# Performance work log

Measured on AMD Instinct MI355X. Metric: run time of the kernel, lower is better.

Reference implementation:

```python
import jax, jax.numpy as jnp
import numpy as np

NH = 8          # n_heads
CLIP = 10.0     # tanh_clipping


def _make_heads(x):
    # (B, n, H) -> (B, NH, n, H//NH)
    B, n, H = x.shape
    return x.reshape(B, n, NH, H // NH).transpose(0, 2, 1, 3)


def setup_inputs() -> dict:
    key = jax.random.key(0)
    ks = jax.random.split(key, 12)
    B, N, G, H = 64, 2000, 128, 128
    s = 1.0 / np.sqrt(H)
    embeddings = jax.random.normal(ks[0], (B, N, H), jnp.float32)
    u = jax.random.uniform(ks[1], (B, G, N))
    group_ninf_mask = jnp.where(u < 0.1, -1e9, 0.0).astype(jnp.float32)
    w = lambda k: (jax.random.normal(k, (H, H), jnp.float32) * s)
    return {
        'embeddings': embeddings,
        'group_ninf_mask': group_ninf_mask,
        'Wq_graph': w(ks[2]), 'Wq_source': w(ks[3]), 'Wq_target': w(ks[4]),
        'Wq_last': w(ks[5]), 'Wk': w(ks[6]), 'Wv': w(ks[7]),
        'Wc': w(ks[8]), 'bc': jnp.zeros((H,), jnp.float32),
        'source_node': jax.random.randint(ks[9], (B,), 0, N),
        'target_node': jax.random.randint(ks[10], (B,), 0, N),
        'last_node': jax.random.randint(ks[11], (B, G), 0, N),
    }


def reference(embeddings, group_ninf_mask, Wq_graph, Wq_source, Wq_target,
              Wq_last, Wk, Wv, Wc, bc, source_node, target_node, last_node):
    B, N, H = embeddings.shape
    G = group_ninf_mask.shape[1]
    hd = H // NH
    b = jnp.arange(B)

    # --- reset() state ---
    graph_emb = embeddings.mean(axis=1, keepdims=True)              # (B,1,H)
    q_graph = _make_heads(graph_emb @ Wq_graph.T)                   # (B,NH,1,hd)
    src_emb = embeddings[b, source_node][:, None, :]                # (B,1,H)
    q_source = _make_heads(src_emb @ Wq_source.T)
    tgt_emb = embeddings[b, target_node][:, None, :]                # (B,1,H)
    q_target = _make_heads(tgt_emb @ Wq_target.T)
    glimpse_k = _make_heads(embeddings @ Wk.T)                      # (B,NH,N,hd)
    glimpse_v = _make_heads(embeddings @ Wv.T)                      # (B,NH,N,hd)

    # --- forward(last_node) ---
    last_emb = embeddings[b[:, None], last_node]                    # (B,G,H)
    q_last = _make_heads(last_emb @ Wq_last.T)                      # (B,NH,G,hd)
    glimpse_q = q_graph + q_source + q_target + q_last              # (B,NH,G,hd)

    scores = jnp.einsum('bhgd,bhnd->bhgn', glimpse_q, glimpse_k) / np.sqrt(hd)
    scores = scores + group_ninf_mask[:, None, :, :]                # mask per head
    attn = jax.nn.softmax(scores, axis=-1)                          # (B,NH,G,N)
    heads = jnp.einsum('bhgn,bhnd->bhgd', attn, glimpse_v)          # (B,NH,G,hd)
    mh_out = heads.transpose(0, 2, 1, 3).reshape(B, G, H)           # (B,G,H)
    final_q = mh_out @ Wc.T + bc                                    # multi_head_combine

    # single-head logits vs logit_k = embeddings^T, tanh-clipped + masked
    logits = jnp.einsum('bgh,bnh->bgn', final_q, embeddings) / np.sqrt(H)
    logits = CLIP * jnp.tanh(logits) + group_ninf_mask
    probs = jax.nn.softmax(logits, axis=2)                          # (B,G,N)
    return probs
```

## Files before the change

### kernel.cpp

```cpp
#include <hip/hip_runtime.h>
#include <hip/hip_bf16.h>

#define BB 64
#define NN 2000
#define GG 128
#define HH 128
#define NHEAD 8
#define HD 16

typedef __attribute__((ext_vector_type(8))) short short8;
typedef __attribute__((ext_vector_type(4))) float f32x4;

__device__ __forceinline__ unsigned short bf16hi(float f) {
    union { float f; unsigned u; } v; v.f = f;
    return (unsigned short)(v.u >> 16);
}
__device__ __forceinline__ float bf16tof(unsigned short h) {
    union { float f; unsigned u; } v; v.u = ((unsigned)h) << 16;
    return v.f;
}

__device__ __forceinline__ void fma8x8(const float4& a0, const float4& a1,
                                       const float4& b0, const float4& b1,
                                       float acc[8][8]) {
    const float av[8] = {a0.x, a0.y, a0.z, a0.w, a1.x, a1.y, a1.z, a1.w};
    const float bv[8] = {b0.x, b0.y, b0.z, b0.w, b1.x, b1.y, b1.z, b1.w};
#pragma unroll
    for (int i = 0; i < 8; ++i)
#pragma unroll
        for (int k = 0; k < 8; ++k) acc[i][k] += av[i] * bv[k];
}

__global__ __launch_bounds__(256) void k_wt(const float* w0, const float* w1, const float* w2,
                     const float* w3, const float* w4, const float* w5,
                     const float* w6, float* WT,
                     unsigned short* Wkhi, unsigned short* Wklo,
                     unsigned short* Wvhi, unsigned short* Wvlo) {
    int m = blockIdx.x;
    if (m >= 5) {
        const float* src = (m == 5) ? w4 : w5;
        unsigned short* dh = (m == 5) ? Wkhi : Wvhi;
        unsigned short* dl = (m == 5) ? Wklo : Wvlo;
        for (int e = threadIdx.x * 4; e < 16384; e += 1024) {
            float4 v = *(const float4*)(src + e);
            float fv[4] = {v.x, v.y, v.z, v.w};
            unsigned short h4[4], l4[4];
#pragma unroll
            for (int i = 0; i < 4; ++i) {
                h4[i] = bf16hi(fv[i]); l4[i] = bf16hi(fv[i] - bf16tof(h4[i]));
            }
            uint2 ph, pl;
            ph.x = h4[0] | (h4[1] << 16); ph.y = h4[2] | (h4[3] << 16);
            pl.x = l4[0] | (l4[1] << 16); pl.y = l4[2] | (l4[3] << 16);
            *(uint2*)(dh + e) = ph;
            *(uint2*)(dl + e) = pl;
        }
        return;
    }
    __shared__ float t[128 * 129];
    const float* src = (m == 0) ? w0 : (m == 1) ? w1 : (m == 2) ? w2 : (m == 3) ? w3 : w6;
    int slot = (m == 4) ? 6 : m;
    for (int e = threadIdx.x; e < 16384; e += 256) {
        int c = e >> 7, j = e & 127;
        t[c * 129 + j] = src[e];
    }
    __syncthreads();
    for (int e = threadIdx.x; e < 16384; e += 256) {
        int j = e >> 7, c = e & 127;
        WT[slot * 16384 + e] = t[c * 129 + j];
    }
}

__global__ __launch_bounds__(256) void k_maskbits(const float* mask, unsigned long long* bits) {
    int bg = blockIdx.x;
    int lane = threadIdx.x & 63;
    int wv = threadIdx.x >> 6;
    for (int w = wv; w < 32; w += 4) {
        int n = w * 64 + lane;
        bool keep = false;
        if (n < NN) keep = (mask[(size_t)bg * NN + n] == 0.0f);
        unsigned long long bal = __ballot(keep);
        if (lane == 0) bits[bg * 32 + w] = bal;
    }
}

__global__ __launch_bounds__(128) void k_gsum(const float* emb, float* gpart) {
    int ck = blockIdx.x, b = blockIdx.y, c = threadIdx.x;
    const float* p = emb + ((size_t)b * NN + ck * 125) * HH + c;
    float s = 0.0f;
#pragma unroll 5
    for (int r = 0; r < 125; ++r) s += p[(size_t)r * HH];
    gpart[ck * 8192 + b * 128 + c] = s;
}

__global__ __launch_bounds__(128) void k_qbase(const float* emb, const int* srcn, const int* tgtn,
                        const float* gpart, const float* WT, float* qbase) {
    int b = blockIdx.x, c = threadIdx.x;
    __shared__ float ge[128], se[128], te[128];
    float s = 0.0f;
#pragma unroll
    for (int t = 0; t < 16; ++t) s += gpart[t * 8192 + b * 128 + c];
    ge[c] = s * (1.0f / 2000.0f);
    se[c] = emb[((size_t)b * NN + srcn[b]) * HH + c];
    te[c] = emb[((size_t)b * NN + tgtn[b]) * HH + c];
    __syncthreads();
    const float* Wg = WT;
    const float* Ws = WT + 16384;
    const float* Wt2 = WT + 32768;
    float acc = 0.0f;
#pragma unroll 4
    for (int j = 0; j < 128; ++j) {
        acc += ge[j] * Wg[j * 128 + c] + se[j] * Ws[j * 128 + c] + te[j] * Wt2[j * 128 + c];
    }
    qbase[b * 128 + c] = acc;
}

__global__ __launch_bounds__(256) void k_qlast(const float* emb, const int* lastn, const float* WT,
                        const float* qbase, unsigned short* Qhi, unsigned short* Qlo) {
    int b = blockIdx.x;
    int tid = threadIdx.x, xq = tid & 15, yq = tid >> 4;
    __shared__ float Bl[128 * 132];
    for (int e = tid; e < 16384; e += 256) {
        int g = e >> 7, j = e & 127;
        Bl[j * 132 + g] = emb[((size_t)b * NN + lastn[b * 128 + g]) * HH + j];
    }
    __syncthreads();
    const float* Wql = WT + 3 * 16384;
    float acc[8][8] = {};
#pragma unroll 4
    for (int j = 0; j < 128; ++j) {
        const float4* Ar = (const float4*)(Wql + j * 128);
        float4 a0 = Ar[yq], a1 = Ar[16 + yq];
        const float4* Br = (const float4*)(Bl + j * 132);
        float4 b0 = Br[xq], b1 = Br[16 + xq];
        fma8x8(a0, a1, b0, b1, acc);
    }
    float4 qb0 = *(const float4*)(qbase + b * 128 + 4 * yq);
    float4 qb1 = *(const float4*)(qbase + b * 128 + 64 + 4 * yq);
    const float q0v[4] = {qb0.x, qb0.y, qb0.z, qb0.w};
    const float q1v[4] = {qb1.x, qb1.y, qb1.z, qb1.w};
#pragma unroll
    for (int k = 0; k < 8; ++k) {
        int g = (k < 4) ? (4 * xq + k) : (64 + 4 * xq + (k - 4));
        size_t base = ((size_t)b * 128 + g) * 128;
        unsigned short h4[4], l4[4];
#pragma unroll
        for (int i = 0; i < 4; ++i) {
            float f = (acc[i][k] + q0v[i]) * 0.25f;
            h4[i] = bf16hi(f); l4[i] = bf16hi(f - bf16tof(h4[i]));
        }
        uint2 ph, pl;
        ph.x = h4[0] | (h4[1] << 16); ph.y = h4[2] | (h4[3] << 16);
        pl.x = l4[0] | (l4[1] << 16); pl.y = l4[2] | (l4[3] << 16);
        *(uint2*)(Qhi + base + 4 * yq) = ph;
        *(uint2*)(Qlo + base + 4 * yq) = pl;
#pragma unroll
        for (int i = 0; i < 4; ++i) {
            float f = (acc[4 + i][k] + q1v[i]) * 0.25f;
            h4[i] = bf16hi(f); l4[i] = bf16hi(f - bf16tof(h4[i]));
        }
        ph.x = h4[0] | (h4[1] << 16); ph.y = h4[2] | (h4[3] << 16);
        pl.x = l4[0] | (l4[1] << 16); pl.y = l4[2] | (l4[3] << 16);
        *(uint2*)(Qhi + base + 64 + 4 * yq) = ph;
        *(uint2*)(Qlo + base + 64 + 4 * yq) = pl;
    }
}

__device__ __forceinline__ void stage_emb(const float* emb, int b, int n0, int tid,
                                          unsigned short (*Eh)[128], unsigned short (*El)[128]) {
    int rr = tid >> 5, c4 = (tid & 31) * 4;
#pragma unroll
    for (int p = 0; p < 16; ++p) {
        int r = p * 8 + rr;
        int n = n0 + r;
        float4 v = make_float4(0.f, 0.f, 0.f, 0.f);
        if (n < NN) v = *(const float4*)(emb + ((size_t)b * NN + n) * HH + c4);
        float fv[4] = {v.x, v.y, v.z, v.w};
        unsigned short h4[4], l4[4];
#pragma unroll
        for (int i = 0; i < 4; ++i) {
            h4[i] = bf16hi(fv[i]); l4[i] = bf16hi(fv[i] - bf16tof(h4[i]));
        }
        uint2 ph, pl;
        ph.x = h4[0] | (h4[1] << 16); ph.y = h4[2] | (h4[3] << 16);
        pl.x = l4[0] | (l4[1] << 16); pl.y = l4[2] | (l4[3] << 16);
        int cs = c4 ^ ((r & 7) << 3);
        *(uint2*)&Eh[r][cs] = ph;
        *(uint2*)&El[r][cs] = pl;
    }
}

__global__ __launch_bounds__(256) void k_kv(const float* emb,
        const unsigned short* Wkhi, const unsigned short* Wklo,
        const unsigned short* Wvhi, const unsigned short* Wvlo,
        unsigned short* Khi, unsigned short* Klo,
        unsigned short* Vhi, unsigned short* Vlo) {
    int nt = blockIdx.x, b = blockIdx.y;
    int tid = threadIdx.x;
    int wv = tid >> 6, lane = tid & 63, l15 = lane & 15, q3 = lane >> 4;
    int n0 = nt * 128;
    __shared__ __align__(16) char ldsbuf[65536];
    unsigned short (*Eh)[128] = (unsigned short(*)[128])ldsbuf;
    unsigned short (*El)[128] = (unsigned short(*)[128])(ldsbuf + 32768);
    stage_emb(emb, b, n0, tid, Eh, El);
    __syncthreads();
    f32x4 aK[2][8], aV[2][8];
#pragma unroll
    for (int t = 0; t < 2; ++t)
#pragma unroll
        for (int ct = 0; ct < 8; ++ct) {
            aK[t][ct] = (f32x4){0.f, 0.f, 0.f, 0.f};
            aV[t][ct] = (f32x4){0.f, 0.f, 0.f, 0.f};
        }
#pragma unroll
    for (int ks = 0; ks < 4; ++ks) {
        short8 eh[2], el[2];
#pragma unroll
        for (int t = 0; t < 2; ++t) {
            int r = wv * 32 + t * 16 + l15;
            int cs = (ks * 32 + q3 * 8) ^ ((r & 7) << 3);
            eh[t] = *(const short8*)&Eh[r][cs];
            el[t] = *(const short8*)&El[r][cs];
        }
#pragma unroll
        for (int ct = 0; ct < 8; ++ct) {
            size_t woff = ((size_t)(ct * 16 + l15)) * 128 + ks * 32 + q3 * 8;
            short8 wkh = *(const short8*)(Wkhi + woff);
            short8 wkl = *(const short8*)(Wklo + woff);
            short8 wvh = *(const short8*)(Wvhi + woff);
            short8 wvl = *(const short8*)(Wvlo + woff);
#pragma unroll
            for (int t = 0; t < 2; ++t) {
                aK[t][ct] = __builtin_amdgcn_mfma_f32_16x16x32_bf16(eh[t], wkh, aK[t][ct], 0, 0, 0);
                aK[t][ct] = __builtin_amdgcn_mfma_f32_16x16x32_bf16(el[t], wkh, aK[t][ct], 0, 0, 0);
                aK[t][ct] = __builtin_amdgcn_mfma_f32_16x16x32_bf16(eh[t], wkl, aK[t][ct], 0, 0, 0);
                aV[t][ct] = __builtin_amdgcn_mfma_f32_16x16x32_bf16(eh[t], wvh, aV[t][ct], 0, 0, 0);
                aV[t][ct] = __builtin_amdgcn_mfma_f32_16x16x32_bf16(el[t], wvh, aV[t][ct], 0, 0, 0);
                aV[t][ct] = __builtin_amdgcn_mfma_f32_16x16x32_bf16(eh[t], wvl, aV[t][ct], 0, 0, 0);
            }
        }
    }
#pragma unroll
    for (int t = 0; t < 2; ++t) {
        int nb = n0 + wv * 32 + t * 16 + 4 * q3;
#pragma unroll
        for (int ct = 0; ct < 8; ++ct) {
            size_t kbase = ((size_t)b * 8 + ct) * 32000 + l15;
#pragma unroll
            for (int r = 0; r < 4; ++r) {
                int n = nb + r;
                if (n < NN) {
                    float f = aK[t][ct][r];
                    unsigned short hh = bf16hi(f);
                    Khi[kbase + (size_t)n * 16] = hh;
                    Klo[kbase + (size_t)n * 16] = bf16hi(f - bf16tof(hh));
                }
            }
            if (nb + 3 < NN) {
                unsigned short h4[4], l4[4];
#pragma unroll
                for (int r = 0; r < 4; ++r) {
                    float f = aV[t][ct][r];
                    h4[r] = bf16hi(f); l4[r] = bf16hi(f - bf16tof(h4[r]));
                }
                uint2 ph, pl;
                ph.x = h4[0] | (h4[1] << 16); ph.y = h4[2] | (h4[3] << 16);
                pl.x = l4[0] | (l4[1] << 16); pl.y = l4[2] | (l4[3] << 16);
                size_t vbase = (((size_t)b * 8 + ct) * 16 + l15) * 2000 + nb;
                *(uint2*)(Vhi + vbase) = ph;
                *(uint2*)(Vlo + vbase) = pl;
            }
        }
    }
}

__global__ __launch_bounds__(256) void k_flash(const unsigned short* Khi, const unsigned short* Klo,
                        const unsigned short* Vhi, const unsigned short* Vlo,
                        const unsigned short* Qhi, const unsigned short* Qlo,
                        const unsigned long long* bits, float* Opart, float* Zpart) {
    int bid = blockIdx.x;
    int s4 = bid & 3, h = (bid >> 2) & 7, b = bid >> 5;
    int tid = threadIdx.x;
    int wv = tid >> 6, lane = tid & 63, l15 = lane & 15, q3 = lane >> 4;

    __shared__ unsigned short Klds[2][64][24];
    __shared__ unsigned short Vlds[2][16][72];
    __shared__ unsigned short Plds[4][2][32][72];

    const short8 z8 = {0, 0, 0, 0, 0, 0, 0, 0};

    short8 qf[2][2];
#pragma unroll
    for (int gt = 0; gt < 2; ++gt) {
        int g = wv * 32 + gt * 16 + l15;
        if (q3 < 2) {
            size_t off = ((size_t)b * 128 + g) * 128 + h * 16 + q3 * 8;
            qf[gt][0] = *(const short8*)(Qhi + off);
            qf[gt][1] = *(const short8*)(Qlo + off);
        } else {
            qf[gt][0] = z8; qf[gt][1] = z8;
        }
    }

    f32x4 Oacc[2] = {{0.f, 0.f, 0.f, 0.f}, {0.f, 0.f, 0.f, 0.f}};
    float zacc[2] = {0.f, 0.f};

    const unsigned long long* bb0 = bits + (((size_t)b * 128 + wv * 32 + l15) * 32);
    const unsigned long long* bb1 = bb0 + 16 * 32;

    size_t kvbase = ((size_t)b * 8 + h);
    const unsigned short* Kh = Khi + kvbase * 2000 * 16;
    const unsigned short* Kl = Klo + kvbase * 2000 * 16;
    const unsigned short* Vh = Vhi + kvbase * 16 * 2000;
    const unsigned short* Vl = Vlo + kvbase * 16 * 2000;

    int snr = tid >> 2, sj4 = (tid & 3) * 4;
    int svd = tid >> 4, svn = (tid & 15) * 4;

    for (int ch = s4 * 8; ch < s4 * 8 + 8; ++ch) {
        int n0 = ch * 64;
        __syncthreads();
        {
            uint2 zz; zz.x = 0; zz.y = 0;
            int n = n0 + snr;
            uint2 k0 = zz, k1 = zz;
            if (n < NN) {
                size_t off = ((size_t)n) * 16 + sj4;
                k0 = *(const uint2*)(Kh + off);
                k1 = *(const uint2*)(Kl + off);
            }
            *(uint2*)&Klds[0][snr][sj4] = k0;
            *(uint2*)&Klds[1][snr][sj4] = k1;
            int vn = n0 + svn;
            uint2 v0 = zz, v1 = zz;
            if (vn + 3 < NN) {
                size_t off = ((size_t)svd) * 2000 + vn;
                v0 = *(const uint2*)(Vh + off);
                v1 = *(const uint2*)(Vl + off);
            }
            *(uint2*)&Vlds[0][svd][svn] = v0;
            *(uint2*)&Vlds[1][svd][svn] = v1;
        }
        __syncthreads();

        unsigned long long wm0 = bb0[ch];
        unsigned long long wm1 = bb1[ch];

        f32x4 S[4][2];
#pragma unroll
        for (int nt = 0; nt < 4; ++nt) {
            short8 kh, kl;
            if (q3 < 2) {
                kh = *(const short8*)&Klds[0][nt * 16 + l15][q3 * 8];
                kl = *(const short8*)&Klds[1][nt * 16 + l15][q3 * 8];
            } else { kh = z8; kl = z8; }
#pragma unroll
            for (int gt = 0; gt < 2; ++gt) {
                f32x4 c = {0.f, 0.f, 0.f, 0.f};
                c = __builtin_amdgcn_mfma_f32_16x16x32_bf16(kh, qf[gt][0], c, 0, 0, 0);
                c = __builtin_amdgcn_mfma_f32_16x16x32_bf16(kh, qf[gt][1], c, 0, 0, 0);
                c = __builtin_amdgcn_mfma_f32_16x16x32_bf16(kl, qf[gt][0], c, 0, 0, 0);
                S[nt][gt] = c;
            }
        }

#pragma unroll
        for (int nt = 0; nt < 4; ++nt) {
#pragma unroll
            for (int gt = 0; gt < 2; ++gt) {
                unsigned long long wm = gt ? wm1 : wm0;
                float p[4];
#pragma unroll
                for (int r = 0; r < 4; ++r) {
                    int sh = nt * 16 + q3 * 4 + r;
                    float e = ((wm >> sh) & 1ull) ? __expf(S[nt][gt][r]) : 0.0f;
                    p[r] = e;
                    zacc[gt] += e;
                }
                unsigned short h4[4], l4[4];
#pragma unroll
                for (int r = 0; r < 4; ++r) {
                    h4[r] = bf16hi(p[r]); l4[r] = bf16hi(p[r] - bf16tof(h4[r]));
                }
                uint2 ph, pl;
                ph.x = h4[0] | (h4[1] << 16); ph.y = h4[2] | (h4[3] << 16);
                pl.x = l4[0] | (l4[1] << 16); pl.y = l4[2] | (l4[3] << 16);
                *(uint2*)&Plds[wv][0][gt * 16 + l15][nt * 16 + q3 * 4] = ph;
                *(uint2*)&Plds[wv][1][gt * 16 + l15][nt * 16 + q3 * 4] = pl;
            }
        }

#pragma unroll
        for (int ks = 0; ks < 2; ++ks) {
            short8 vh = *(const short8*)&Vlds[0][l15][ks * 32 + q3 * 8];
            short8 vl = *(const short8*)&Vlds[1][l15][ks * 32 + q3 * 8];
#pragma unroll
            for (int gt = 0; gt < 2; ++gt) {
                short8 ph = *(const short8*)&Plds[wv][0][gt * 16 + l15][ks * 32 + q3 * 8];
                short8 pl = *(const short8*)&Plds[wv][1][gt * 16 + l15][ks * 32 + q3 * 8];
                Oacc[gt] = __builtin_amdgcn_mfma_f32_16x16x32_bf16(vh, ph, Oacc[gt], 0, 0, 0);
                Oacc[gt] = __builtin_amdgcn_mfma_f32_16x16x32_bf16(vh, pl, Oacc[gt], 0, 0, 0);
                Oacc[gt] = __builtin_amdgcn_mfma_f32_16x16x32_bf16(vl, ph, Oacc[gt], 0, 0, 0);
            }
        }
    }

    size_t obase = (((size_t)s4 * 64 + b) * 8 + h);
#pragma unroll
    for (int gt = 0; gt < 2; ++gt) {
        float z = zacc[gt];
        z += __shfl_xor(z, 16);
        z += __shfl_xor(z, 32);
        int g = wv * 32 + gt * 16 + l15;
        if (q3 == 0) Zpart[obase * 128 + g] = z;
#pragma unroll
        for (int r = 0; r < 4; ++r) {
            int d = q3 * 4 + r;
            Opart[(obase * 16 + d) * 128 + g] = Oacc[gt][r];
        }
    }
}

__global__ __launch_bounds__(256) void k_ocomb(const float* Opart, const float* Zpart, float* MHt) {
    int bh = blockIdx.x;
    int b = bh >> 3, h = bh & 7;
    int tid = threadIdx.x;
    for (int e = tid; e < 2048; e += 256) {
        int d = e >> 7, g = e & 127;
        float z = 0.0f, o = 0.0f;
#pragma unroll
        for (int s = 0; s < 4; ++s) {
            z += Zpart[(((size_t)s * 64 + b) * 8 + h) * 128 + g];
            o += Opart[((((size_t)s * 64 + b) * 8 + h) * 16 + d) * 128 + g];
        }
        MHt[((size_t)b * 128 + h * 16 + d) * 128 + g] = o / z;
    }
}

__global__ __launch_bounds__(256) void k_fq(const float* MHt, const float* WT, const float* bcv,
                                            unsigned short* FQhi, unsigned short* FQlo) {
    int b = blockIdx.x;
    int tid = threadIdx.x, xq = tid & 15, yq = tid >> 4;
    __shared__ float Bl[128 * 132];
    for (int e = tid; e < 16384; e += 256) {
        int j = e >> 7, g = e & 127;
        Bl[j * 132 + g] = MHt[(size_t)b * 16384 + e];
    }
    __syncthreads();
    const float* Wc = WT + 6 * 16384;
    float acc[8][8] = {};
#pragma unroll 4
    for (int j = 0; j < 128; ++j) {
        const float4* Ar = (const float4*)(Wc + j * 128);
        float4 a0 = Ar[yq], a1 = Ar[16 + yq];
        const float4* Br = (const float4*)(Bl + j * 132);
        float4 b0 = Br[xq], b1 = Br[16 + xq];
        fma8x8(a0, a1, b0, b1, acc);
    }
    float4 bc0 = *(const float4*)(bcv + 4 * yq);
    float4 bc1 = *(const float4*)(bcv + 64 + 4 * yq);
    const float bcv8[8] = {bc0.x, bc0.y, bc0.z, bc0.w, bc1.x, bc1.y, bc1.z, bc1.w};
    const float sc = 0.08838834764831845f;
#pragma unroll
    for (int k = 0; k < 8; ++k) {
        int g = (k < 4) ? (4 * xq + k) : (64 + 4 * xq + (k - 4));
        size_t base = ((size_t)b * 128 + g) * 128;
        unsigned short h4[4], l4[4];
#pragma unroll
        for (int i = 0; i < 4; ++i) {
            float f = (acc[i][k] + bcv8[i]) * sc;
            h4[i] = bf16hi(f); l4[i] = bf16hi(f - bf16tof(h4[i]));
        }
        uint2 ph, pl;
        ph.x = h4[0] | (h4[1] << 16); ph.y = h4[2] | (h4[3] << 16);
        pl.x = l4[0] | (l4[1] << 16); pl.y = l4[2] | (l4[3] << 16);
        *(uint2*)(FQhi + base + 4 * yq) = ph;
        *(uint2*)(FQlo + base + 4 * yq) = pl;
#pragma unroll
        for (int i = 0; i < 4; ++i) {
            float f = (acc[4 + i][k] + bcv8[4 + i]) * sc;
            h4[i] = bf16hi(f); l4[i] = bf16hi(f - bf16tof(h4[i]));
        }
        ph.x = h4[0] | (h4[1] << 16); ph.y = h4[2] | (h4[3] << 16);
        pl.x = l4[0] | (l4[1] << 16); pl.y = l4[2] | (l4[3] << 16);
        *(uint2*)(FQhi + base + 64 + 4 * yq) = ph;
        *(uint2*)(FQlo + base + 64 + 4 * yq) = pl;
    }
}

__global__ __launch_bounds__(256) void k_logits(const float* emb,
        const unsigned short* FQhi, const unsigned short* FQlo,
        const unsigned long long* bits, float* out, float* Zp) {
    int nt = blockIdx.x, b = blockIdx.y;
    int tid = threadIdx.x;
    int wv = tid >> 6, lane = tid & 63, l15 = lane & 15, q3 = lane >> 4;
    int n0 = nt * 128;
    __shared__ __align__(16) char ldsbuf[65536];
    unsigned short (*Eh)[128] = (unsigned short(*)[128])ldsbuf;
    unsigned short (*El)[128] = (unsigned short(*)[128])(ldsbuf + 32768);
    float (*Pl)[128] = (float(*)[128])ldsbuf;
    stage_emb(emb, b, n0, tid, Eh, El);
    __syncthreads();
    f32x4 acc[2][8];
#pragma unroll
    for (int t = 0; t < 2; ++t)
#pragma unroll
        for (int gt = 0; gt < 8; ++gt) acc[t][gt] = (f32x4){0.f, 0.f, 0.f, 0.f};
#pragma unroll
    for (int ks = 0; ks < 4; ++ks) {
        short8 beh[2], bel[2];
#pragma unroll
        for (int t = 0; t < 2; ++t) {
            int r = wv * 32 + t * 16 + l15;
            int cs = (ks * 32 + q3 * 8) ^ ((r & 7) << 3);
            beh[t] = *(const short8*)&Eh[r][cs];
            bel[t] = *(const short8*)&El[r][cs];
        }
#pragma unroll
        for (int gt = 0; gt < 8; ++gt) {
            size_t foff = ((size_t)b * 128 + gt * 16 + l15) * 128 + ks * 32 + q3 * 8;
            short8 fh = *(const short8*)(FQhi + foff);
            short8 fl = *(const short8*)(FQlo + foff);
#pragma unroll
            for (int t = 0; t < 2; ++t) {
                acc[t][gt] = __builtin_amdgcn_mfma_f32_16x16x32_bf16(fh, beh[t], acc[t][gt], 0, 0, 0);
                acc[t][gt] = __builtin_amdgcn_mfma_f32_16x16x32_bf16(fl, beh[t], acc[t][gt], 0, 0, 0);
                acc[t][gt] = __builtin_amdgcn_mfma_f32_16x16x32_bf16(fh, bel[t], acc[t][gt], 0, 0, 0);
            }
        }
    }
    __syncthreads();
    float psum[8][4];
#pragma unroll
    for (int gt = 0; gt < 8; ++gt)
#pragma unroll
        for (int r = 0; r < 4; ++r) psum[gt][r] = 0.f;
    const unsigned long long* bb = bits + (size_t)b * 128 * 32;
#pragma unroll
    for (int t = 0; t < 2; ++t) {
        int nl = wv * 32 + t * 16 + l15;
        int wordofs = nt * 2 + ((wv * 32 + t * 16) >> 6);
        int sh = (n0 + nl) & 63;
#pragma unroll
        for (int gt = 0; gt < 8; ++gt) {
#pragma unroll
            for (int r = 0; r < 4; ++r) {
                int g = gt * 16 + 4 * q3 + r;
                unsigned long long wm = bb[g * 32 + wordofs];
                float l = acc[t][gt][r];
                float e2 = __expf(2.0f * l);
                float th = 1.0f - 2.0f / (e2 + 1.0f);
                float p = ((wm >> sh) & 1ull) ? __expf(10.0f * th) : 0.0f;
                psum[gt][r] += p;
                Pl[g][nl ^ ((g & 7) << 2)] = p;
            }
        }
    }
#pragma unroll
    for (int gt = 0; gt < 8; ++gt)
#pragma unroll
        for (int r = 0; r < 4; ++r) {
            float v = psum[gt][r];
            v += __shfl_xor(v, 1); v += __shfl_xor(v, 2);
            v += __shfl_xor(v, 4); v += __shfl_xor(v, 8);
            if (l15 == 0) {
                int g = gt * 16 + 4 * q3 + r;
                Zp[((size_t)(nt * 4 + wv)) * 8192 + b * 128 + g] = v;
            }
        }
    __syncthreads();
    for (int e = tid; e < 4096; e += 256) {
        int g = e >> 5, c4 = (e & 31) * 4;
        int n = n0 + c4;
        if (n + 3 < NN) {
            *(float4*)(out + ((size_t)b * 128 + g) * NN + n) =
                *(float4*)&Pl[g][c4 ^ ((g & 7) << 2)];
        }
    }
}

__global__ __launch_bounds__(256) void k_norm(const float* Zp, float* out) {
    int bg = blockIdx.x;
    __shared__ float invs;
    if (threadIdx.x == 0) {
        float s = 0.0f;
#pragma unroll
        for (int t = 0; t < 64; ++t) s += Zp[(size_t)t * 8192 + bg];
        invs = 1.0f / s;
    }
    __syncthreads();
    float inv = invs;
    for (int n = threadIdx.x; n < NN; n += 256) out[(size_t)bg * NN + n] *= inv;
}

extern "C" void kernel_launch(void* const* d_in, const int* in_sizes, int n_in,
                              void* d_out, int out_size, void* d_ws, size_t ws_size,
                              hipStream_t stream) {
    const float* emb = (const float*)d_in[0];
    const float* mask = (const float*)d_in[1];
    const float* Wqg = (const float*)d_in[2];
    const float* Wqs = (const float*)d_in[3];
    const float* Wqt = (const float*)d_in[4];
    const float* Wql = (const float*)d_in[5];
    const float* Wk = (const float*)d_in[6];
    const float* Wv = (const float*)d_in[7];
    const float* Wc = (const float*)d_in[8];
    const float* bc = (const float*)d_in[9];
    const int* srcn = (const int*)d_in[10];
    const int* tgtn = (const int*)d_in[11];
    const int* lastn = (const int*)d_in[12];
    float* out = (float*)d_out;

    float* ws = (float*)d_ws;
    float* WT = ws;
    unsigned short* Wkhi = (unsigned short*)(WT + 4 * 16384);
    unsigned short* Wklo = Wkhi + 16384;
    unsigned short* Wvhi = Wklo + 16384;
    unsigned short* Wvlo = Wvhi + 16384;
    float* gpart = ws + 114688;
    float* qbase = ws + 245760;
    float* MHt = ws + 253952;
    unsigned short* FQhi = (unsigned short*)(ws + 1302528);
    unsigned short* FQlo = FQhi + 1048576;
    float* Zp = ws + 2351104;
    unsigned short* Khi = (unsigned short*)(ws + 2875392);
    unsigned short* Klo = (unsigned short*)(ws + 11067392);
    unsigned short* Vhi = (unsigned short*)(ws + 19259392);
    unsigned short* Vlo = (unsigned short*)(ws + 27451392);
    unsigned long long* bits = (unsigned long long*)(ws + 35643392);

    float* Opart = out;
    float* Zpart = out + 4194304;
    unsigned short* Qhi = (unsigned short*)(out + 4456448);
    unsigned short* Qlo = Qhi + 1048576;

    k_wt<<<7, 256, 0, stream>>>(Wqg, Wqs, Wqt, Wql, Wk, Wv, Wc, WT, Wkhi, Wklo, Wvhi, Wvlo);
    k_maskbits<<<8192, 256, 0, stream>>>(mask, bits);
    k_gsum<<<dim3(16, 64), 128, 0, stream>>>(emb, gpart);
    k_kv<<<dim3(16, 64), 256, 0, stream>>>(emb, Wkhi, Wklo, Wvhi, Wvlo, Khi, Klo, Vhi, Vlo);
    k_qbase<<<64, 128, 0, stream>>>(emb, srcn, tgtn, gpart, WT, qbase);
    k_qlast<<<64, 256, 0, stream>>>(emb, lastn, WT, qbase, Qhi, Qlo);
    k_flash<<<2048, 256, 0, stream>>>(Khi, Klo, Vhi, Vlo, Qhi, Qlo, bits, Opart, Zpart);
    k_ocomb<<<512, 256, 0, stream>>>(Opart, Zpart, MHt);
    k_fq<<<64, 256, 0, stream>>>(MHt, WT, bc, FQhi, FQlo);
    k_logits<<<dim3(16, 64), 256, 0, stream>>>(emb, FQhi, FQlo, bits, out, Zp);
    k_norm<<<8192, 256, 0, stream>>>(Zp, out);
}
```

Before: 415.1 us.

## Halve node tiles in kv/logits and stage K/V stores through LDS for coalescing

The k_kv and k_logits kernels now process 64 nodes per block instead of 128, doubling the grid to 32x64 and cutting LDS use to 36KB so more blocks fit per CU. In k_kv the K and V results are transposed through LDS and written to global memory as 16-byte vector stores, replacing scattered 2-byte K stores. The Zp partial-sum buffer grows to 128 slices, so k_norm sums more partials and the workspace offsets shift. In exchange there are extra LDS round trips and barriers, and each weight/FQ tile loaded from global memory is reused over fewer nodes.

Result: slower. 496.1 us (+19.5%).

```diff
diff --git a/kernel.cpp b/kernel.cpp
--- a/kernel.cpp
+++ b/kernel.cpp
@@ -166,11 +166,11 @@
     }
 }
 
-__device__ __forceinline__ void stage_emb(const float* emb, int b, int n0, int tid,
-                                          unsigned short (*Eh)[128], unsigned short (*El)[128]) {
+__device__ __forceinline__ void stage_emb64(const float* emb, int b, int n0, int tid,
+                                            unsigned short (*Eh)[128], unsigned short (*El)[128]) {
     int rr = tid >> 5, c4 = (tid & 31) * 4;
 #pragma unroll
-    for (int p = 0; p < 16; ++p) {
+    for (int p = 0; p < 8; ++p) {
         int r = p * 8 + rr;
         int n = n0 + r;
         float4 v = make_float4(0.f, 0.f, 0.f, 0.f);
@@ -198,30 +198,30 @@
     int nt = blockIdx.x, b = blockIdx.y;
     int tid = threadIdx.x;
     int wv = tid >> 6, lane = tid & 63, l15 = lane & 15, q3 = lane >> 4;
-    int n0 = nt * 128;
-    __shared__ __align__(16) char ldsbuf[65536];
+    int n0 = nt * 64;
+    __shared__ __align__(16) char ldsbuf[36864];
     unsigned short (*Eh)[128] = (unsigned short(*)[128])ldsbuf;
-    unsigned short (*El)[128] = (unsigned short(*)[128])(ldsbuf + 32768);
-    stage_emb(emb, b, n0, tid, Eh, El);
-    __syncthreads();
-    f32x4 aK[2][8], aV[2][8];
-#pragma unroll
-    for (int t = 0; t < 2; ++t)
-#pragma unroll
-        for (int ct = 0; ct < 8; ++ct) {
-            aK[t][ct] = (f32x4){0.f, 0.f, 0.f, 0.f};
-            aV[t][ct] = (f32x4){0.f, 0.f, 0.f, 0.f};
-        }
+    unsigned short (*El)[128] = (unsigned short(*)[128])(ldsbuf + 16384);
+    unsigned short (*Kth)[136] = (unsigned short(*)[136])ldsbuf;
+    unsigned short (*Ktl)[136] = (unsigned short(*)[136])(ldsbuf + 17408);
+    unsigned short (*Vth)[72] = (unsigned short(*)[72])ldsbuf;
+    unsigned short (*Vtl)[72] = (unsigned short(*)[72])(ldsbuf + 18432);
+
+    stage_emb64(emb, b, n0, tid, Eh, El);
+    __syncthreads();
+
+    f32x4 aK[8], aV[8];
+#pragma unroll
+    for (int ct = 0; ct < 8; ++ct) {
+        aK[ct] = (f32x4){0.f, 0.f, 0.f, 0.f};
+        aV[ct] = (f32x4){0.f, 0.f, 0.f, 0.f};
+    }
+    int rA = wv * 16 + l15;
 #pragma unroll
     for (int ks = 0; ks < 4; ++ks) {
-        short8 eh[2], el[2];
-#pragma unroll
-        for (int t = 0; t < 2; ++t) {
-            int r = wv * 32 + t * 16 + l15;
-            int cs = (ks * 32 + q3 * 8) ^ ((r & 7) << 3);
-            eh[t] = *(const short8*)&Eh[r][cs];
-            el[t] = *(const short8*)&El[r][cs];
-        }
+        int cs = (ks * 32 + q3 * 8) ^ ((rA & 7) << 3);
+        short8 eh = *(const short8*)&Eh[rA][cs];
+        short8 el = *(const short8*)&El[rA][cs];
 #pragma unroll
         for (int ct = 0; ct < 8; ++ct) {
             size_t woff = ((size_t)(ct * 16 + l15)) * 128 + ks * 32 + q3 * 8;
@@ -229,47 +229,75 @@
             short8 wkl = *(const short8*)(Wklo + woff);
             short8 wvh = *(const short8*)(Wvhi + woff);
             short8 wvl = *(const short8*)(Wvlo + woff);
-#pragma unroll
-            for (int t = 0; t < 2; ++t) {
-                aK[t][ct] = __builtin_amdgcn_mfma_f32_16x16x32_bf16(eh[t], wkh, aK[t][ct], 0, 0, 0);
-                aK[t][ct] = __builtin_amdgcn_mfma_f32_16x16x32_bf16(el[t], wkh, aK[t][ct], 0, 0, 0);
-                aK[t][ct] = __builtin_amdgcn_mfma_f32_16x16x32_bf16(eh[t], wkl, aK[t][ct], 0, 0, 0);
-                aV[t][ct] = __builtin_amdgcn_mfma_f32_16x16x32_bf16(eh[t], wvh, aV[t][ct], 0, 0, 0);
-                aV[t][ct] = __builtin_amdgcn_mfma_f32_16x16x32_bf16(el[t], wvh, aV[t][ct], 0, 0, 0);
-                aV[t][ct] = __builtin_amdgcn_mfma_f32_16x16x32_bf16(eh[t], wvl, aV[t][ct], 0, 0, 0);
-            }
-        }
-    }
-#pragma unroll
-    for (int t = 0; t < 2; ++t) {
-        int nb = n0 + wv * 32 + t * 16 + 4 * q3;
-#pragma unroll
-        for (int ct = 0; ct < 8; ++ct) {
-            size_t kbase = ((size_t)b * 8 + ct) * 32000 + l15;
-#pragma unroll
-            for (int r = 0; r < 4; ++r) {
-                int n = nb + r;
-                if (n < NN) {
-                    float f = aK[t][ct][r];
-                    unsigned short hh = bf16hi(f);
-                    Khi[kbase + (size_t)n * 16] = hh;
-                    Klo[kbase + (size_t)n * 16] = bf16hi(f - bf16tof(hh));
-                }
-            }
-            if (nb + 3 < NN) {
-                unsigned short h4[4], l4[4];
-#pragma unroll
-                for (int r = 0; r < 4; ++r) {
-                    float f = aV[t][ct][r];
-                    h4[r] = bf16hi(f); l4[r] = bf16hi(f - bf16tof(h4[r]));
-                }
-                uint2 ph, pl;
-                ph.x = h4[0] | (h4[1] << 16); ph.y = h4[2] | (h4[3] << 16);
-                pl.x = l4[0] | (l4[1] << 16); pl.y = l4[2] | (l4[3] << 16);
-                size_t vbase = (((size_t)b * 8 + ct) * 16 + l15) * 2000 + nb;
-                *(uint2*)(Vhi + vbase) = ph;
-                *(uint2*)(Vlo + vbase) = pl;
-            }
+            aK[ct] = __builtin_amdgcn_mfma_f32_16x16x32_bf16(eh, wkh, aK[ct], 0, 0, 0);
+            aK[ct] = __builtin_amdgcn_mfma_f32_16x16x32_bf16(el, wkh, aK[ct], 0, 0, 0);
+            aK[ct] = __builtin_amdgcn_mfma_f32_16x16x32_bf16(eh, wkl, aK[ct], 0, 0, 0);
+            aV[ct] = __builtin_amdgcn_mfma_f32_16x16x32_bf16(eh, wvh, aV[ct], 0, 0, 0);
+            aV[ct] = __builtin_amdgcn_mfma_f32_16x16x32_bf16(el, wvh, aV[ct], 0, 0, 0);
+            aV[ct] = __builtin_amdgcn_mfma_f32_16x16x32_bf16(eh, wvl, aV[ct], 0, 0, 0);
+        }
+    }
+    __syncthreads();
+    int nl0 = wv * 16 + 4 * q3;
+#pragma unroll
+    for (int ct = 0; ct < 8; ++ct) {
+        int c = ct * 16 + l15;
+#pragma unroll
+        for (int r = 0; r < 4; ++r) {
+            float f = aK[ct][r];
+            unsigned short hh = bf16hi(f);
+            Kth[nl0 + r][c] = hh;
+            Ktl[nl0 + r][c] = bf16hi(f - bf16tof(hh));
+        }
+    }
+    __syncthreads();
+#pragma unroll
+    for (int p = 0; p < 8; ++p) {
+        int e = p * 256 + tid;
+        int half = e >> 10;
+        int e2 = e & 1023;
+        int h = e2 >> 7;
+        int rem = e2 & 127;
+        int n = rem >> 1;
+        int d8 = (rem & 1) * 8;
+        if (n0 + n < NN) {
+            uint4 v = half ? *(const uint4*)&Ktl[n][h * 16 + d8]
+                           : *(const uint4*)&Kth[n][h * 16 + d8];
+            unsigned short* dst = (half ? Klo : Khi) +
+                (((size_t)b * 8 + h) * 2000 + n0 + n) * 16 + d8;
+            *(uint4*)dst = v;
+        }
+    }
+    __syncthreads();
+#pragma unroll
+    for (int ct = 0; ct < 8; ++ct) {
+        int c = ct * 16 + l15;
+        unsigned short h4[4], l4[4];
+#pragma unroll
+        for (int r = 0; r < 4; ++r) {
+            float f = aV[ct][r];
+            h4[r] = bf16hi(f); l4[r] = bf16hi(f - bf16tof(h4[r]));
+        }
+        uint2 ph, pl;
+        ph.x = h4[0] | (h4[1] << 16); ph.y = h4[2] | (h4[3] << 16);
+        pl.x = l4[0] | (l4[1] << 16); pl.y = l4[2] | (l4[3] << 16);
+        *(uint2*)&Vth[c][nl0] = ph;
+        *(uint2*)&Vtl[c][nl0] = pl;
+    }
+    __syncthreads();
+#pragma unroll
+    for (int p = 0; p < 8; ++p) {
+        int e = p * 256 + tid;
+        int half = e >> 10;
+        int e2 = e & 1023;
+        int c = e2 >> 3;
+        int n8 = (e2 & 7) * 8;
+        if (n0 + n8 + 7 < NN) {
+            uint4 v = half ? *(const uint4*)&Vtl[c][n8]
+                           : *(const uint4*)&Vth[c][n8];
+            unsigned short* dst = (half ? Vlo : Vhi) +
+                ((size_t)b * 128 + c) * 2000 + n0 + n8;
+            *(uint4*)dst = v;
         }
     }
 }
@@ -494,39 +522,30 @@
     int nt = blockIdx.x, b = blockIdx.y;
     int tid = threadIdx.x;
     int wv = tid >> 6, lane = tid & 63, l15 = lane & 15, q3 = lane >> 4;
-    int n0 = nt * 128;
-    __shared__ __align__(16) char ldsbuf[65536];
+    int n0 = nt * 64;
+    __shared__ __align__(16) char ldsbuf[36864];
     unsigned short (*Eh)[128] = (unsigned short(*)[128])ldsbuf;
-    unsigned short (*El)[128] = (unsigned short(*)[128])(ldsbuf + 32768);
-    float (*Pl)[128] = (float(*)[128])ldsbuf;
-    stage_emb(emb, b, n0, tid, Eh, El);
-    __syncthreads();
-    f32x4 acc[2][8];
-#pragma unroll
-    for (int t = 0; t < 2; ++t)
-#pragma unroll
-        for (int gt = 0; gt < 8; ++gt) acc[t][gt] = (f32x4){0.f, 0.f, 0.f, 0.f};
+    unsigned short (*El)[128] = (unsigned short(*)[128])(ldsbuf + 16384);
+    float (*Pl)[68] = (float(*)[68])ldsbuf;
+    stage_emb64(emb, b, n0, tid, Eh, El);
+    __syncthreads();
+    f32x4 acc[8];
+#pragma unroll
+    for (int gt = 0; gt < 8; ++gt) acc[gt] = (f32x4){0.f, 0.f, 0.f, 0.f};
+    int rB = wv * 16 + l15;
 #pragma unroll
     for (int ks = 0; ks < 4; ++ks) {
-        short8 beh[2], bel[2];
-#pragma unroll
-        for (int t = 0; t < 2; ++t) {
-            int r = wv * 32 + t * 16 + l15;
-            int cs = (ks * 32 + q3 * 8) ^ ((r & 7) << 3);
-            beh[t] = *(const short8*)&Eh[r][cs];
-            bel[t] = *(const short8*)&El[r][cs];
-        }
+        int cs = (ks * 32 + q3 * 8) ^ ((rB & 7) << 3);
+        short8 beh = *(const short8*)&Eh[rB][cs];
+        short8 bel = *(const short8*)&El[rB][cs];
 #pragma unroll
         for (int gt = 0; gt < 8; ++gt) {
             size_t foff = ((size_t)b * 128 + gt * 16 + l15) * 128 + ks * 32 + q3 * 8;
             short8 fh = *(const short8*)(FQhi + foff);
             short8 fl = *(const short8*)(FQlo + foff);
-#pragma unroll
-            for (int t = 0; t < 2; ++t) {
-                acc[t][gt] = __builtin_amdgcn_mfma_f32_16x16x32_bf16(fh, beh[t], acc[t][gt], 0, 0, 0);
-                acc[t][gt] = __builtin_amdgcn_mfma_f32_16x16x32_bf16(fl, beh[t], acc[t][gt], 0, 0, 0);
-                acc[t][gt] = __builtin_amdgcn_mfma_f32_16x16x32_bf16(fh, bel[t], acc[t][gt], 0, 0, 0);
-            }
+            acc[gt] = __builtin_amdgcn_mfma_f32_16x16x32_bf16(fh, beh, acc[gt], 0, 0, 0);
+            acc[gt] = __builtin_amdgcn_mfma_f32_16x16x32_bf16(fl, beh, acc[gt], 0, 0, 0);
+            acc[gt] = __builtin_amdgcn_mfma_f32_16x16x32_bf16(fh, bel, acc[gt], 0, 0, 0);
         }
     }
     __syncthreads();
@@ -536,24 +555,19 @@
 #pragma unroll
         for (int r = 0; r < 4; ++r) psum[gt][r] = 0.f;
     const unsigned long long* bb = bits + (size_t)b * 128 * 32;
-#pragma unroll
-    for (int t = 0; t < 2; ++t) {
-        int nl = wv * 32 + t * 16 + l15;
-        int wordofs = nt * 2 + ((wv * 32 + t * 16) >> 6);
-        int sh = (n0 + nl) & 63;
-#pragma unroll
-        for (int gt = 0; gt < 8; ++gt) {
-#pragma unroll
-            for (int r = 0; r < 4; ++r) {
-                int g = gt * 16 + 4 * q3 + r;
-                unsigned long long wm = bb[g * 32 + wordofs];
-                float l = acc[t][gt][r];
-                float e2 = __expf(2.0f * l);
-                float th = 1.0f - 2.0f / (e2 + 1.0f);
-                float p = ((wm >> sh) & 1ull) ? __expf(10.0f * th) : 0.0f;
-                psum[gt][r] += p;
-                Pl[g][nl ^ ((g & 7) << 2)] = p;
-            }
+    int nl = wv * 16 + l15;
+#pragma unroll
+    for (int gt = 0; gt < 8; ++gt) {
+#pragma unroll
+        for (int r = 0; r < 4; ++r) {
+            int g = gt * 16 + 4 * q3 + r;
+            unsigned long long wm = bb[g * 32 + nt];
+            float l = acc[gt][r];
+            float e2 = __expf(2.0f * l);
+            float th = 1.0f - 2.0f / (e2 + 1.0f);
+            float p = ((wm >> nl) & 1ull) ? __expf(10.0f * th) : 0.0f;
+            psum[gt][r] += p;
+            Pl[g][nl] = p;
         }
     }
 #pragma unroll
@@ -569,12 +583,11 @@
             }
         }
     __syncthreads();
-    for (int e = tid; e < 4096; e += 256) {
-        int g = e >> 5, c4 = (e & 31) * 4;
+    for (int e = tid; e < 2048; e += 256) {
+        int g = e >> 4, c4 = (e & 15) * 4;
         int n = n0 + c4;
         if (n + 3 < NN) {
-            *(float4*)(out + ((size_t)b * 128 + g) * NN + n) =
-                *(float4*)&Pl[g][c4 ^ ((g & 7) << 2)];
+            *(float4*)(out + ((size_t)b * 128 + g) * NN + n) = *(float4*)&Pl[g][c4];
         }
     }
 }
@@ -585,7 +598,7 @@
     if (threadIdx.x == 0) {
         float s = 0.0f;
 #pragma unroll
-        for (int t = 0; t < 64; ++t) s += Zp[(size_t)t * 8192 + bg];
+        for (int t = 0; t < 128; ++t) s += Zp[(size_t)t * 8192 + bg];
         invs = 1.0f / s;
     }
     __syncthreads();
@@ -623,11 +636,11 @@
     unsigned short* FQhi = (unsigned short*)(ws + 1302528);
     unsigned short* FQlo = FQhi + 1048576;
     float* Zp = ws + 2351104;
-    unsigned short* Khi = (unsigned short*)(ws + 2875392);
-    unsigned short* Klo = (unsigned short*)(ws + 11067392);
-    unsigned short* Vhi = (unsigned short*)(ws + 19259392);
-    unsigned short* Vlo = (unsigned short*)(ws + 27451392);
-    unsigned long long* bits = (unsigned long long*)(ws + 35643392);
+    unsigned short* Khi = (unsigned short*)(ws + 3399680);
+    unsigned short* Klo = (unsigned short*)(ws + 11591680);
+    unsigned short* Vhi = (unsigned short*)(ws + 19783680);
+    unsigned short* Vlo = (unsigned short*)(ws + 27975680);
+    unsigned long long* bits = (unsigned long long*)(ws + 36167680);
 
     float* Opart = out;
     float* Zpart = out + 4194304;
@@ -637,12 +650,12 @@
     k_wt<<<7, 256, 0, stream>>>(Wqg, Wqs, Wqt, Wql, Wk, Wv, Wc, WT, Wkhi, Wklo, Wvhi, Wvlo);
     k_maskbits<<<8192, 256, 0, stream>>>(mask, bits);
     k_gsum<<<dim3(16, 64), 128, 0, stream>>>(emb, gpart);
-    k_kv<<<dim3(16, 64), 256, 0, stream>>>(emb, Wkhi, Wklo, Wvhi, Wvlo, Khi, Klo, Vhi, Vlo);
+    k_kv<<<dim3(32, 64), 256, 0, stream>>>(emb, Wkhi, Wklo, Wvhi, Wvlo, Khi, Klo, Vhi, Vlo);
     k_qbase<<<64, 128, 0, stream>>>(emb, srcn, tgtn, gpart, WT, qbase);
     k_qlast<<<64, 256, 0, stream>>>(emb, lastn, WT, qbase, Qhi, Qlo);
     k_flash<<<2048, 256, 0, stream>>>(Khi, Klo, Vhi, Vlo, Qhi, Qlo, bits, Opart, Zpart);
     k_ocomb<<<512, 256, 0, stream>>>(Opart, Zpart, MHt);
     k_fq<<<64, 256, 0, stream>>>(MHt, WT, bc, FQhi, FQlo);
-    k_logits<<<dim3(16, 64), 256, 0, stream>>>(emb, FQhi, FQlo, bits, out, Zp);
+    k_logits<<<dim3(32, 64), 256, 0, stream>>>(emb, FQhi, FQlo, bits, out, Zp);
     k_norm<<<8192, 256, 0, stream>>>(Zp, out);
 }
```

## Load embeddings directly into MFMA fragments and drop LDS staging in k_kv/k_logits

Applied to the files above, without the earlier changes.

k_kv and k_logits no longer stage the embedding tile as bf16 hi/lo in 64KB of shared memory. Each lane now loads its own rows straight from global memory into MFMA operand registers. The loops are reordered so the output-column tile is outermost with small per-tile accumulators. k_logits also writes the probabilities directly from registers instead of transposing through LDS for coalesced float4 stores. The goal is to cut LDS footprint and barriers to raise occupancy, at the cost of narrower 64-byte output write segments and more register pressure. Workspace offsets for the K, V and mask-bit buffers are shifted.

New measurement: 365.6 us. 11.9% less time.

```diff
diff --git a/kernel.cpp b/kernel.cpp
--- a/kernel.cpp
+++ b/kernel.cpp
@@ -18,6 +18,17 @@
 __device__ __forceinline__ float bf16tof(unsigned short h) {
     union { float f; unsigned u; } v; v.u = ((unsigned)h) << 16;
     return v.f;
+}
+
+__device__ __forceinline__ void cvt8(const float4& v0, const float4& v1,
+                                     short8& hi, short8& lo) {
+    float fv[8] = {v0.x, v0.y, v0.z, v0.w, v1.x, v1.y, v1.z, v1.w};
+#pragma unroll
+    for (int i = 0; i < 8; ++i) {
+        unsigned short h = bf16hi(fv[i]);
+        hi[i] = (short)h;
+        lo[i] = (short)bf16hi(fv[i] - bf16tof(h));
+    }
 }
 
 __device__ __forceinline__ void fma8x8(const float4& a0, const float4& a1,
@@ -166,30 +177,6 @@
     }
 }
 
-__device__ __forceinline__ void stage_emb(const float* emb, int b, int n0, int tid,
-                                          unsigned short (*Eh)[128], unsigned short (*El)[128]) {
-    int rr = tid >> 5, c4 = (tid & 31) * 4;
-#pragma unroll
-    for (int p = 0; p < 16; ++p) {
-        int r = p * 8 + rr;
-        int n = n0 + r;
-        float4 v = make_float4(0.f, 0.f, 0.f, 0.f);
-        if (n < NN) v = *(const float4*)(emb + ((size_t)b * NN + n) * HH + c4);
-        float fv[4] = {v.x, v.y, v.z, v.w};
-        unsigned short h4[4], l4[4];
-#pragma unroll
-        for (int i = 0; i < 4; ++i) {
-            h4[i] = bf16hi(fv[i]); l4[i] = bf16hi(fv[i] - bf16tof(h4[i]));
-        }
-        uint2 ph, pl;
-        ph.x = h4[0] | (h4[1] << 16); ph.y = h4[2] | (h4[3] << 16);
-        pl.x = l4[0] | (l4[1] << 16); pl.y = l4[2] | (l4[3] << 16);
-        int cs = c4 ^ ((r & 7) << 3);
-        *(uint2*)&Eh[r][cs] = ph;
-        *(uint2*)&El[r][cs] = pl;
-    }
-}
-
 __global__ __launch_bounds__(256) void k_kv(const float* emb,
         const unsigned short* Wkhi, const unsigned short* Wklo,
         const unsigned short* Wvhi, const unsigned short* Wvlo,
@@ -199,31 +186,30 @@
     int tid = threadIdx.x;
     int wv = tid >> 6, lane = tid & 63, l15 = lane & 15, q3 = lane >> 4;
     int n0 = nt * 128;
-    __shared__ __align__(16) char ldsbuf[65536];
-    unsigned short (*Eh)[128] = (unsigned short(*)[128])ldsbuf;
-    unsigned short (*El)[128] = (unsigned short(*)[128])(ldsbuf + 32768);
-    stage_emb(emb, b, n0, tid, Eh, El);
-    __syncthreads();
-    f32x4 aK[2][8], aV[2][8];
-#pragma unroll
-    for (int t = 0; t < 2; ++t)
-#pragma unroll
-        for (int ct = 0; ct < 8; ++ct) {
-            aK[t][ct] = (f32x4){0.f, 0.f, 0.f, 0.f};
-            aV[t][ct] = (f32x4){0.f, 0.f, 0.f, 0.f};
-        }
-#pragma unroll
-    for (int ks = 0; ks < 4; ++ks) {
-        short8 eh[2], el[2];
-#pragma unroll
-        for (int t = 0; t < 2; ++t) {
-            int r = wv * 32 + t * 16 + l15;
-            int cs = (ks * 32 + q3 * 8) ^ ((r & 7) << 3);
-            eh[t] = *(const short8*)&Eh[r][cs];
-            el[t] = *(const short8*)&El[r][cs];
-        }
-#pragma unroll
-        for (int ct = 0; ct < 8; ++ct) {
+
+    short8 eh[2][4], el[2][4];
+#pragma unroll
+    for (int t = 0; t < 2; ++t) {
+        int n = n0 + wv * 32 + t * 16 + l15;
+        const float* rowp = emb + ((size_t)b * NN + n) * HH + q3 * 8;
+        bool ok = (n < NN);
+#pragma unroll
+        for (int ks = 0; ks < 4; ++ks) {
+            float4 v0 = make_float4(0.f, 0.f, 0.f, 0.f), v1 = v0;
+            if (ok) {
+                v0 = *(const float4*)(rowp + ks * 32);
+                v1 = *(const float4*)(rowp + ks * 32 + 4);
+            }
+            cvt8(v0, v1, eh[t][ks], el[t][ks]);
+        }
+    }
+
+#pragma unroll
+    for (int ct = 0; ct < 8; ++ct) {
+        f32x4 aK[2] = {{0.f, 0.f, 0.f, 0.f}, {0.f, 0.f, 0.f, 0.f}};
+        f32x4 aV[2] = {{0.f, 0.f, 0.f, 0.f}, {0.f, 0.f, 0.f, 0.f}};
+#pragma unroll
+        for (int ks = 0; ks < 4; ++ks) {
             size_t woff = ((size_t)(ct * 16 + l15)) * 128 + ks * 32 + q3 * 8;
             short8 wkh = *(const short8*)(Wkhi + woff);
             short8 wkl = *(const short8*)(Wklo + woff);
@@ -231,26 +217,23 @@
             short8 wvl = *(const short8*)(Wvlo + woff);
 #pragma unroll
             for (int t = 0; t < 2; ++t) {
-                aK[t][ct] = __builtin_amdgcn_mfma_f32_16x16x32_bf16(eh[t], wkh, aK[t][ct], 0, 0, 0);
-                aK[t][ct] = __builtin_amdgcn_mfma_f32_16x16x32_bf16(el[t], wkh, aK[t][ct], 0, 0, 0);
-                aK[t][ct] = __builtin_amdgcn_mfma_f32_16x16x32_bf16(eh[t], wkl, aK[t][ct], 0, 0, 0);
-                aV[t][ct] = __builtin_amdgcn_mfma_f32_16x16x32_bf16(eh[t], wvh, aV[t][ct], 0, 0, 0);
-                aV[t][ct] = __builtin_amdgcn_mfma_f32_16x16x32_bf16(el[t], wvh, aV[t][ct], 0, 0, 0);
-                aV[t][ct] = __builtin_amdgcn_mfma_f32_16x16x32_bf16(eh[t], wvl, aV[t][ct], 0, 0, 0);
-            }
-        }
-    }
-#pragma unroll
-    for (int t = 0; t < 2; ++t) {
-        int nb = n0 + wv * 32 + t * 16 + 4 * q3;
-#pragma unroll
-        for (int ct = 0; ct < 8; ++ct) {
+                aK[t] = __builtin_amdgcn_mfma_f32_16x16x32_bf16(eh[t][ks], wkh, aK[t], 0, 0, 0);
+                aK[t] = __builtin_amdgcn_mfma_f32_16x16x32_bf16(el[t][ks], wkh, aK[t], 0, 0, 0);
+                aK[t] = __builtin_amdgcn_mfma_f32_16x16x32_bf16(eh[t][ks], wkl, aK[t], 0, 0, 0);
+                aV[t] = __builtin_amdgcn_mfma_f32_16x16x32_bf16(eh[t][ks], wvh, aV[t], 0, 0, 0);
+                aV[t] = __builtin_amdgcn_mfma_f32_16x16x32_bf16(el[t][ks], wvh, aV[t], 0, 0, 0);
+                aV[t] = __builtin_amdgcn_mfma_f32_16x16x32_bf16(eh[t][ks], wvl, aV[t], 0, 0, 0);
+            }
+        }
+#pragma unroll
+        for (int t = 0; t < 2; ++t) {
+            int nb = n0 + wv * 32 + t * 16 + 4 * q3;
             size_t kbase = ((size_t)b * 8 + ct) * 32000 + l15;
 #pragma unroll
             for (int r = 0; r < 4; ++r) {
                 int n = nb + r;
                 if (n < NN) {
-                    float f = aK[t][ct][r];
+                    float f = aK[t][r];
                     unsigned short hh = bf16hi(f);
                     Khi[kbase + (size_t)n * 16] = hh;
                     Klo[kbase + (size_t)n * 16] = bf16hi(f - bf16tof(hh));
@@ -260,7 +243,7 @@
                 unsigned short h4[4], l4[4];
 #pragma unroll
                 for (int r = 0; r < 4; ++r) {
-                    float f = aV[t][ct][r];
+                    float f = aV[t][r];
                     h4[r] = bf16hi(f); l4[r] = bf16hi(f - bf16tof(h4[r]));
                 }
                 uint2 ph, pl;
@@ -495,86 +478,67 @@
     int tid = threadIdx.x;
     int wv = tid >> 6, lane = tid & 63, l15 = lane & 15, q3 = lane >> 4;
     int n0 = nt * 128;
-    __shared__ __align__(16) char ldsbuf[65536];
-    unsigned short (*Eh)[128] = (unsigned short(*)[128])ldsbuf;
-    unsigned short (*El)[128] = (unsigned short(*)[128])(ldsbuf + 32768);
-    float (*Pl)[128] = (float(*)[128])ldsbuf;
-    stage_emb(emb, b, n0, tid, Eh, El);
-    __syncthreads();
-    f32x4 acc[2][8];
-#pragma unroll
-    for (int t = 0; t < 2; ++t)
-#pragma unroll
-        for (int gt = 0; gt < 8; ++gt) acc[t][gt] = (f32x4){0.f, 0.f, 0.f, 0.f};
-#pragma unroll
-    for (int ks = 0; ks < 4; ++ks) {
-        short8 beh[2], bel[2];
-#pragma unroll
-        for (int t = 0; t < 2; ++t) {
-            int r = wv * 32 + t * 16 + l15;
-            int cs = (ks * 32 + q3 * 8) ^ ((r & 7) << 3);
-            beh[t] = *(const short8*)&Eh[r][cs];
-            bel[t] = *(const short8*)&El[r][cs];
-        }
-#pragma unroll
-        for (int gt = 0; gt < 8; ++gt) {
+
+    short8 beh[2][4], bel[2][4];
+#pragma unroll
+    for (int t = 0; t < 2; ++t) {
+        int n = n0 + wv * 32 + t * 16 + l15;
+        const float* rowp = emb + ((size_t)b * NN + n) * HH + q3 * 8;
+        bool ok = (n < NN);
+#pragma unroll
+        for (int ks = 0; ks < 4; ++ks) {
+            float4 v0 = make_float4(0.f, 0.f, 0.f, 0.f), v1 = v0;
+            if (ok) {
+                v0 = *(const float4*)(rowp + ks * 32);
+                v1 = *(const float4*)(rowp + ks * 32 + 4);
+            }
+            cvt8(v0, v1, beh[t][ks], bel[t][ks]);
+        }
+    }
+
+    const unsigned long long* bb = bits + (size_t)b * 128 * 32;
+#pragma unroll
+    for (int gt = 0; gt < 8; ++gt) {
+        f32x4 acc[2] = {{0.f, 0.f, 0.f, 0.f}, {0.f, 0.f, 0.f, 0.f}};
+#pragma unroll
+        for (int ks = 0; ks < 4; ++ks) {
             size_t foff = ((size_t)b * 128 + gt * 16 + l15) * 128 + ks * 32 + q3 * 8;
             short8 fh = *(const short8*)(FQhi + foff);
             short8 fl = *(const short8*)(FQlo + foff);
 #pragma unroll
             for (int t = 0; t < 2; ++t) {
-                acc[t][gt] = __builtin_amdgcn_mfma_f32_16x16x32_bf16(fh, beh[t], acc[t][gt], 0, 0, 0);
-                acc[t][gt] = __builtin_amdgcn_mfma_f32_16x16x32_bf16(fl, beh[t], acc[t][gt], 0, 0, 0);
-                acc[t][gt] = __builtin_amdgcn_mfma_f32_16x16x32_bf16(fh, bel[t], acc[t][gt], 0, 0, 0);
-            }
-        }
-    }
-    __syncthreads();
-    float psum[8][4];
-#pragma unroll
-    for (int gt = 0; gt < 8; ++gt)
-#pragma unroll
-        for (int r = 0; r < 4; ++r) psum[gt][r] = 0.f;
-    const unsigned long long* bb = bits + (size_t)b * 128 * 32;
-#pragma unroll
-    for (int t = 0; t < 2; ++t) {
-        int nl = wv * 32 + t * 16 + l15;
-        int wordofs = nt * 2 + ((wv * 32 + t * 16) >> 6);
-        int sh = (n0 + nl) & 63;
-#pragma unroll
-        for (int gt = 0; gt < 8; ++gt) {
+                acc[t] = __builtin_amdgcn_mfma_f32_16x16x32_bf16(fh, beh[t][ks], acc[t], 0, 0, 0);
+                acc[t] = __builtin_amdgcn_mfma_f32_16x16x32_bf16(fl, beh[t][ks], acc[t], 0, 0, 0);
+                acc[t] = __builtin_amdgcn_mfma_f32_16x16x32_bf16(fh, bel[t][ks], acc[t], 0, 0, 0);
+            }
+        }
+        float psum[4] = {0.f, 0.f, 0.f, 0.f};
+#pragma unroll
+        for (int t = 0; t < 2; ++t) {
+            int n = n0 + wv * 32 + t * 16 + l15;
+            int word = (n0 + wv * 32 + t * 16) >> 6;
+            int sh = n & 63;
 #pragma unroll
             for (int r = 0; r < 4; ++r) {
                 int g = gt * 16 + 4 * q3 + r;
-                unsigned long long wm = bb[g * 32 + wordofs];
-                float l = acc[t][gt][r];
+                unsigned long long wm = bb[g * 32 + word];
+                float l = acc[t][r];
                 float e2 = __expf(2.0f * l);
                 float th = 1.0f - 2.0f / (e2 + 1.0f);
                 float p = ((wm >> sh) & 1ull) ? __expf(10.0f * th) : 0.0f;
-                psum[gt][r] += p;
-                Pl[g][nl ^ ((g & 7) << 2)] = p;
-            }
-        }
-    }
-#pragma unroll
-    for (int gt = 0; gt < 8; ++gt)
+                psum[r] += p;
+                if (n < NN) out[((size_t)b * 128 + g) * NN + n] = p;
+            }
+        }
 #pragma unroll
         for (int r = 0; r < 4; ++r) {
-            float v = psum[gt][r];
+            float v = psum[r];
             v += __shfl_xor(v, 1); v += __shfl_xor(v, 2);
             v += __shfl_xor(v, 4); v += __shfl_xor(v, 8);
             if (l15 == 0) {
                 int g = gt * 16 + 4 * q3 + r;
                 Zp[((size_t)(nt * 4 + wv)) * 8192 + b * 128 + g] = v;
             }
-        }
-    __syncthreads();
-    for (int e = tid; e < 4096; e += 256) {
-        int g = e >> 5, c4 = (e & 31) * 4;
-        int n = n0 + c4;
-        if (n + 3 < NN) {
-            *(float4*)(out + ((size_t)b * 128 + g) * NN + n) =
-                *(float4*)&Pl[g][c4 ^ ((g & 7) << 2)];
         }
     }
 }
@@ -623,11 +587,11 @@
     unsigned short* FQhi = (unsigned short*)(ws + 1302528);
     unsigned short* FQlo = FQhi + 1048576;
     float* Zp = ws + 2351104;
-    unsigned short* Khi = (unsigned short*)(ws + 2875392);
-    unsigned short* Klo = (unsigned short*)(ws + 11067392);
-    unsigned short* Vhi = (unsigned short*)(ws + 19259392);
-    unsigned short* Vlo = (unsigned short*)(ws + 27451392);
-    unsigned long long* bits = (unsigned long long*)(ws + 35643392);
+    unsigned short* Khi = (unsigned short*)(ws + 3399680);
+    unsigned short* Klo = (unsigned short*)(ws + 11591680);
+    unsigned short* Vhi = (unsigned short*)(ws + 19783680);
+    unsigned short* Vlo = (unsigned short*)(ws + 27975680);
+    unsigned long long* bits = (unsigned long long*)(ws + 36167680);
 
     float* Opart = out;
     float* Zpart = out + 4194304;
```
